# Kernel tuning notes

Hardware: AMD Instinct MI355X
Metric: run time of the kernel (lower is better)

The kernel has to match this reference:

```python
import jax, jax.numpy as jnp
import numpy as np

B, S, HID = 2, 2048, 2048
NH, NKV, HD = 16, 4, 128
GROUPS = NH // NKV
ROPE_BASE = 10000.0


def setup_inputs() -> dict:
    key = jax.random.key(0)
    ks = jax.random.split(key, 12)

    def w(k, i, o):
        return (jax.random.normal(k, (i, o), jnp.float32) * (i ** -0.5)).astype(jnp.float32)

    return {
        'x_real': jax.random.normal(ks[0], (B, S, HID), jnp.float32),
        'x_imag': jax.random.normal(ks[1], (B, S, HID), jnp.float32),
        'Wq_r': w(ks[2], HID, HID), 'Wq_i': w(ks[3], HID, HID),
        'bq_r': jnp.zeros((HID,), jnp.float32), 'bq_i': jnp.zeros((HID,), jnp.float32),
        'Wk_r': w(ks[4], HID, NKV * HD), 'Wk_i': w(ks[5], HID, NKV * HD),
        'bk_r': jnp.zeros((NKV * HD,), jnp.float32), 'bk_i': jnp.zeros((NKV * HD,), jnp.float32),
        'Wv_r': w(ks[6], HID, NKV * HD), 'Wv_i': w(ks[7], HID, NKV * HD),
        'bv_r': jnp.zeros((NKV * HD,), jnp.float32), 'bv_i': jnp.zeros((NKV * HD,), jnp.float32),
        'Wo_r': w(ks[8], HID, HID), 'Wo_i': w(ks[9], HID, HID),
        'bo_r': jnp.zeros((HID,), jnp.float32), 'bo_i': jnp.zeros((HID,), jnp.float32),
    }


def _clinear(xr, xi, Wr, Wi, br, bi):
    # complex linear: (xr + i*xi) @ (Wr + i*Wi) + (br + i*bi)
    out_r = xr @ Wr - xi @ Wi + br
    out_i = xr @ Wi + xi @ Wr + bi
    return out_r, out_i


def _split_heads(xr, xi, n_heads):
    b, s, _ = xr.shape
    xr = xr.reshape(b, s, n_heads, -1).transpose(0, 2, 1, 3)  # [B,H,S,D]
    xi = xi.reshape(b, s, n_heads, -1).transpose(0, 2, 1, 3)
    return xr, xi


def _rope(xr, xi):
    # complex rotary embedding: multiply (xr + i*xi) by exp(i * pos * inv_freq)
    s, d = xr.shape[-2], xr.shape[-1]
    inv_freq = 1.0 / (ROPE_BASE ** (jnp.arange(0, d, 2, dtype=jnp.float32) / d))
    freqs = jnp.arange(s, dtype=jnp.float32)[:, None] * inv_freq[None, :]  # [S, D/2]
    emb = jnp.concatenate([freqs, freqs], axis=-1)  # [S, D]
    cos, sin = jnp.cos(emb), jnp.sin(emb)
    return xr * cos - xi * sin, xr * sin + xi * cos


def _repeat_kv(xr, xi):
    if GROUPS == 1:
        return xr, xi
    b, hkv, s, d = xr.shape
    xr = jnp.broadcast_to(xr[:, :, None], (b, hkv, GROUPS, s, d)).reshape(b, NH, s, d)
    xi = jnp.broadcast_to(xi[:, :, None], (b, hkv, GROUPS, s, d)).reshape(b, NH, s, d)
    return xr, xi


def reference(x_real, x_imag, Wq_r, Wq_i, bq_r, bq_i, Wk_r, Wk_i, bk_r, bk_i,
              Wv_r, Wv_i, bv_r, bv_i, Wo_r, Wo_i, bo_r, bo_i):
    q_r, q_i = _clinear(x_real, x_imag, Wq_r, Wq_i, bq_r, bq_i)
    k_r, k_i = _clinear(x_real, x_imag, Wk_r, Wk_i, bk_r, bk_i)
    v_r, v_i = _clinear(x_real, x_imag, Wv_r, Wv_i, bv_r, bv_i)

    q_r, q_i = _split_heads(q_r, q_i, NH)
    k_r, k_i = _split_heads(k_r, k_i, NKV)
    v_r, v_i = _split_heads(v_r, v_i, NKV)

    q_r, q_i = _rope(q_r, q_i)
    k_r, k_i = _rope(k_r, k_i)

    k_r, k_i = _repeat_kv(k_r, k_i)
    v_r, v_i = _repeat_kv(v_r, v_i)

    scale = 1.0 / jnp.sqrt(jnp.float32(HD))
    # real part of complex inner product q . conj(k)
    scores = (jnp.einsum('bhqd,bhkd->bhqk', q_r, k_r)
              + jnp.einsum('bhqd,bhkd->bhqk', q_i, k_i)) * scale
    s = scores.shape[-1]
    causal = jnp.tril(jnp.ones((s, s), bool))
    scores = jnp.where(causal, scores, jnp.float32(-1e9))
    attn = jax.nn.softmax(scores, axis=-1)  # [B,H,S,S]

    out_r = jnp.einsum('bhqk,bhkd->bhqd', attn, v_r)
    out_i = jnp.einsum('bhqk,bhkd->bhqd', attn, v_i)

    # merge heads
    b = out_r.shape[0]
    out_r = out_r.transpose(0, 2, 1, 3).reshape(b, s, NH * HD)
    out_i = out_i.transpose(0, 2, 1, 3).reshape(b, s, NH * HD)

    out_r, out_i = _clinear(out_r, out_i, Wo_r, Wo_i, bo_r, bo_i)
    return out_r, out_i, attn
```

## Files before the change

kernel.cpp:

```cpp
#include <hip/hip_runtime.h>
#include <hip/hip_bf16.h>

#define S_LEN 2048
#define HIDDEN 2048
#define NHEAD 16
#define NKVH 4
#define HEADD 128
#define BATCH 2

typedef __attribute__((ext_vector_type(4))) float f32x4;
typedef __attribute__((ext_vector_type(8))) short bf16x8;
typedef __attribute__((ext_vector_type(4))) unsigned short u16x4;

__device__ __forceinline__ unsigned short f2bf(float f) {
  union { __hip_bfloat16 h; unsigned short u; } cv;
  cv.h = __float2bfloat16(f);
  return cv.u;
}

__device__ __forceinline__ float bf2f(unsigned short u) {
  union { float f; unsigned int i; } cv;
  cv.i = (unsigned int)u << 16;
  return cv.f;
}

__device__ __forceinline__ void gl_lds16(const void* g, void* l) {
  __builtin_amdgcn_global_load_lds(
      (const __attribute__((address_space(1))) unsigned int*)g,
      (__attribute__((address_space(3))) unsigned int*)l,
      16, 0, 0);
}

__device__ __forceinline__ f32x4 mfma16(bf16x8 a, bf16x8 b, f32x4 c) {
  return __builtin_amdgcn_mfma_f32_16x16x32_bf16(a, b, c, 0, 0, 0);
}

__global__ void k_rope_table(float* tab) {
  int idx = blockIdx.x * blockDim.x + threadIdx.x;
  if (idx >= S_LEN * 64) return;
  int s = idx >> 6, j = idx & 63;
  float invf = expf(-(float)j * (logf(10000.0f) / 64.0f));
  float ang = (float)s * invf;
  float sn, cs;
  sincosf(ang, &sn, &cs);
  tab[idx * 2 + 0] = cs;
  tab[idx * 2 + 1] = sn;
}

__global__ void k_pack_x(const float* __restrict__ xr, const float* __restrict__ xi,
                         unsigned short* __restrict__ Xp) {
  int idx = blockIdx.x * blockDim.x + threadIdx.x;
  if (idx >= 4096 * 4096 / 4) return;
  int m = idx >> 10;
  int c4 = idx & 1023;
  const float* src = (c4 < 512) ? (xr + (size_t)m * 2048 + c4 * 4)
                                : (xi + (size_t)m * 2048 + (c4 - 512) * 4);
  f32x4 v = *(const f32x4*)src;
  ((u16x4*)Xp)[idx] = (u16x4){f2bf(v.x), f2bf(v.y), f2bf(v.z), f2bf(v.w)};
}

__global__ void k_pack_w(const float* __restrict__ wq_r, const float* __restrict__ wq_i,
                         const float* __restrict__ wk_r, const float* __restrict__ wk_i,
                         const float* __restrict__ wv_r, const float* __restrict__ wv_i,
                         const float* __restrict__ wo_r, const float* __restrict__ wo_i,
                         unsigned short* __restrict__ Wt) {
  __shared__ float tile[32][33];
  int k0 = blockIdx.x * 32;
  int n0 = blockIdx.y * 32;
  int tx = threadIdx.x, ty0 = threadIdx.y;
#pragma unroll
  for (int i = 0; i < 4; ++i) {
    int ty = ty0 + i * 8;
    int k = k0 + ty;
    int n = n0 + tx;
    const float* Wr; const float* Wi; int w, part, j;
    if (n < 4096) {
      Wr = wq_r; Wi = wq_i; w = 2048;
      int h = n >> 8, p = (n >> 7) & 1, d = n & 127;
      part = p; j = h * 128 + d;
    } else if (n < 5120) {
      Wr = wk_r; Wi = wk_i; w = 512;
      int t = n - 4096;
      int kv = t >> 8, p = (t >> 7) & 1, d = t & 127;
      part = p; j = kv * 128 + d;
    } else if (n < 6144) {
      Wr = wv_r; Wi = wv_i; w = 512;
      int t = n - 5120;
      int kv = t >> 8, p = (t >> 7) & 1, d = t & 127;
      part = p; j = kv * 128 + d;
    } else {
      Wr = wo_r; Wi = wo_i; w = 2048;
      int t = n - 6144;
      part = (t >= w); j = part ? (t - w) : t;
    }
    float v;
    if (part == 0) v = (k < 2048) ? Wr[(size_t)k * w + j] : -Wi[(size_t)(k - 2048) * w + j];
    else           v = (k < 2048) ? Wi[(size_t)k * w + j] :  Wr[(size_t)(k - 2048) * w + j];
    tile[ty][tx] = v;
  }
  __syncthreads();
#pragma unroll
  for (int i = 0; i < 4; ++i) {
    int ty = ty0 + i * 8;
    Wt[(size_t)(n0 + ty) * 4096 + k0 + tx] = f2bf(tile[tx][ty]);
  }
}

template <int MODE>
__global__ __launch_bounds__(512, 2) void k_gemm256(
    const unsigned short* __restrict__ A, const unsigned short* __restrict__ Bt,
    int NTN,
    float* __restrict__ outR, float* __restrict__ outI,
    const float* __restrict__ bR, const float* __restrict__ bI,
    const float* __restrict__ tab,
    const float* __restrict__ bqr, const float* __restrict__ bqi,
    const float* __restrict__ bkr, const float* __restrict__ bki,
    const float* __restrict__ bvr, const float* __restrict__ bvi,
    unsigned short* __restrict__ Qcat, unsigned short* __restrict__ Kcat,
    unsigned short* __restrict__ VtP) {
  constexpr int KD = 4096;
  constexpr int Kb = KD * 2;
  constexpr int NT = KD / 64;
  constexpr int NITER = NT / 2;
  __shared__ __align__(16) char smem[131072];
  int tid = threadIdx.x, lane = tid & 63, wid = tid >> 6;
  int wm = wid >> 2, wn = wid & 3;
  int nwg = gridDim.x;
  int bid = blockIdx.x;
  int swz = (bid & 7) * (nwg >> 3) + (bid >> 3);
  int mt = swz / NTN, nt = swz - mt * NTN;
  int m0 = mt * 256, n0 = nt * 256;

  const char* Ab = (const char*)A + (size_t)m0 * Kb;
  const char* Bb = (const char*)Bt + (size_t)n0 * Kb;
  char* L = smem;

  int i0 = tid, i1 = tid + 512;
  int pl0 = (i0 >> 3) * Kb + (((i0 & 7) ^ ((i0 >> 3) & 7)) << 4);
  int pl1 = (i1 >> 3) * Kb + (((i1 & 7) ^ ((i1 >> 3) & 7)) << 4);

  int jx0 = (((lane >> 4)) ^ (lane & 7)) << 4;
  int jx1 = (((lane >> 4) + 4) ^ (lane & 7)) << 4;
  int arow = (wm * 64 + (lane & 15)) * 128;
  int brow = (wn * 32 + (lane & 15)) * 128;

  auto STAGE_A = [&](int buf, int half, int kt) {
    const char* s = Ab + (size_t)half * 128 * Kb + kt * 128;
    char* d = L + buf * 32768 + half * 16384 + (wid << 10);
    gl_lds16(s + pl0, d);
    gl_lds16(s + pl1, d + 8192);
  };
  auto STAGE_B = [&](int buf, int half, int kt) {
    const char* s = Bb + (size_t)half * 128 * Kb + kt * 128;
    char* d = L + 65536 + buf * 32768 + half * 16384 + (wid << 10);
    gl_lds16(s + pl0, d);
    gl_lds16(s + pl1, d + 8192);
  };
  auto LD_A = [&](bf16x8* dst, int buf, int half) {
    const char* base = L + buf * 32768 + half * 16384 + arow;
#pragma unroll
    for (int mf = 0; mf < 4; ++mf) {
      dst[mf * 2 + 0] = *(const bf16x8*)(base + mf * 2048 + jx0);
      dst[mf * 2 + 1] = *(const bf16x8*)(base + mf * 2048 + jx1);
    }
  };
  auto LD_B = [&](bf16x8* dst, int buf, int half) {
    const char* base = L + 65536 + buf * 32768 + half * 16384 + brow;
#pragma unroll
    for (int nf = 0; nf < 2; ++nf) {
      dst[nf * 2 + 0] = *(const bf16x8*)(base + nf * 2048 + jx0);
      dst[nf * 2 + 1] = *(const bf16x8*)(base + nf * 2048 + jx1);
    }
  };

  f32x4 acc[8][4];
  const f32x4 fz = {0.f, 0.f, 0.f, 0.f};
#pragma unroll
  for (int i = 0; i < 8; ++i)
#pragma unroll
    for (int j = 0; j < 4; ++j) acc[i][j] = fz;

  bf16x8 aX[8], aY[8], bX[4], bY[4];

#define BARR() __builtin_amdgcn_s_barrier()
#define WAITV(drain) do { if (drain) asm volatile("s_waitcnt vmcnt(0)" ::: "memory"); \
                          else       asm volatile("s_waitcnt vmcnt(6)" ::: "memory"); } while (0)
#define MMQ(aS, bS, qm, qn) do { \
    __builtin_amdgcn_s_setprio(1); \
    _Pragma("unroll") \
    for (int mf = 0; mf < 4; ++mf) \
      _Pragma("unroll") \
      for (int nf = 0; nf < 2; ++nf) { \
        acc[(qm)*4+mf][(qn)*2+nf] = mfma16(aS[mf*2+0], bS[nf*2+0], acc[(qm)*4+mf][(qn)*2+nf]); \
        acc[(qm)*4+mf][(qn)*2+nf] = mfma16(aS[mf*2+1], bS[nf*2+1], acc[(qm)*4+mf][(qn)*2+nf]); \
      } \
    __builtin_amdgcn_s_setprio(0); \
  } while (0)

  STAGE_A(0, 0, 0);
  STAGE_B(0, 0, 0);
  STAGE_B(0, 1, 0);
  STAGE_A(0, 1, 0);
  STAGE_A(1, 0, 1);
  STAGE_B(1, 0, 1);
  STAGE_B(1, 1, 1);
  asm volatile("s_waitcnt vmcnt(6)" ::: "memory");
  BARR();

  for (int it = 0; it < NITER; ++it) {
    int t1 = 2 * it + 1, t2 = 2 * it + 2, t3 = 2 * it + 3;
    bool nl = (it < NITER - 1);
    LD_A(aX, 0, 0); LD_B(bX, 0, 0);
    STAGE_A(1, 1, t1);
    BARR(); MMQ(aX, bX, 0, 0); BARR();
    LD_B(bY, 0, 1);
    if (nl) STAGE_A(0, 0, t2);
    BARR(); MMQ(aX, bY, 0, 1); BARR();
    LD_A(aY, 0, 1);
    if (nl) STAGE_B(0, 0, t2);
    BARR(); MMQ(aY, bY, 1, 1); BARR();
    if (nl) STAGE_B(0, 1, t2);
    WAITV(!nl); BARR(); MMQ(aY, bX, 1, 0); BARR();
    LD_A(aX, 1, 0); LD_B(bY, 1, 0);
    if (nl) STAGE_A(0, 1, t2);
    BARR(); MMQ(aX, bY, 0, 0); BARR();
    LD_B(bX, 1, 1);
    if (nl) STAGE_A(1, 0, t3);
    BARR(); MMQ(aX, bX, 0, 1); BARR();
    LD_A(aY, 1, 1);
    if (nl) STAGE_B(1, 0, t3);
    BARR(); MMQ(aY, bX, 1, 1); BARR();
    if (nl) STAGE_B(1, 1, t3);
    WAITV(!nl); BARR(); MMQ(aY, bY, 1, 0); BARR();
  }

  int r0 = (lane >> 4) << 2, col0 = lane & 15;

  if (MODE == 1) {
#pragma unroll
    for (int qm = 0; qm < 2; ++qm)
#pragma unroll
      for (int mf = 0; mf < 4; ++mf)
#pragma unroll
        for (int qn = 0; qn < 2; ++qn)
#pragma unroll
          for (int nf = 0; nf < 2; ++nf) {
            f32x4 v = acc[qm * 4 + mf][qn * 2 + nf];
            int rowb = m0 + qm * 128 + wm * 64 + mf * 16 + r0;
            int col = n0 + qn * 128 + wn * 32 + nf * 16 + col0;
#pragma unroll
            for (int r = 0; r < 4; ++r) {
              int row = rowb + r;
              if (col < 2048) outR[(size_t)row * 2048 + col] = v[r] + bR[col];
              else            outI[(size_t)row * 2048 + (col - 2048)] = v[r] + bI[col - 2048];
            }
          }
    return;
  }

  __syncthreads();
  int bidx = m0 >> 11;
  int s0 = m0 & 2047;

  if (n0 < 5120) {
    bool isQ = (n0 < 4096);
    int hh = isQ ? (n0 >> 8) : ((n0 - 4096) >> 8);
    const float* bRp = isQ ? bqr : bkr;
    const float* bIp = isQ ? bqi : bki;
    int jbase = hh * 128;
#pragma unroll
    for (int qm = 0; qm < 2; ++qm)
#pragma unroll
      for (int mf = 0; mf < 4; ++mf)
#pragma unroll
        for (int nf = 0; nf < 2; ++nf) {
          int d = wn * 32 + nf * 16 + col0;
          f32x4 vr = acc[qm * 4 + mf][0 * 2 + nf];
          f32x4 vi = acc[qm * 4 + mf][1 * 2 + nf];
          float br = bRp[jbase + d], bi = bIp[jbase + d];
#pragma unroll
          for (int r = 0; r < 4; ++r) {
            int lrow = qm * 128 + wm * 64 + mf * 16 + r0 + r;
            int s = s0 + lrow;
            float2 cs = *(const float2*)(tab + ((size_t)s * 64 + (d & 63)) * 2);
            float qr = vr[r] + br;
            float qi = vi[r] + bi;
            float orr = qr * cs.x - qi * cs.y;
            float oii = qr * cs.y + qi * cs.x;
            int swz4 = (lrow & 3) << 3;
            int g0 = (d >> 3) ^ swz4;
            int g1 = ((128 + d) >> 3) ^ swz4;
            *(unsigned short*)(L + lrow * 512 + g0 * 16 + (d & 7) * 2) = f2bf(orr);
            *(unsigned short*)(L + lrow * 512 + g1 * 16 + (d & 7) * 2) = f2bf(oii);
          }
        }
    __syncthreads();
    char* dstb = isQ ? (char*)Qcat + ((size_t)(bidx * 16 + hh) * 2048 + s0) * 512
                     : (char*)Kcat + ((size_t)(bidx * 4 + hh) * 2048 + s0) * 512;
#pragma unroll
    for (int i = 0; i < 16; ++i) {
      int cid = tid + 512 * i;
      int row = cid >> 5, c = cid & 31;
      int g = c ^ ((row & 3) << 3);
      *(f32x4*)(dstb + (size_t)row * 512 + c * 16) = *(const f32x4*)(L + row * 512 + g * 16);
    }
  } else {
    int kv = (n0 - 5120) >> 8;
#pragma unroll
    for (int qm = 0; qm < 2; ++qm)
#pragma unroll
      for (int mf = 0; mf < 4; ++mf)
#pragma unroll
        for (int qn = 0; qn < 2; ++qn)
#pragma unroll
          for (int nf = 0; nf < 2; ++nf) {
            int dloc = wn * 32 + nf * 16 + col0;
            int nlocal = qn * 128 + dloc;
            f32x4 v = acc[qm * 4 + mf][qn * 2 + nf];
            float bias = (qn ? bvi : bvr)[kv * 128 + dloc];
#pragma unroll
            for (int r = 0; r < 4; ++r) {
              int lrow = qm * 128 + wm * 64 + mf * 16 + r0 + r;
              int g = (lrow >> 3) ^ (nlocal & 31);
              *(unsigned short*)(L + nlocal * 512 + g * 16 + (lrow & 7) * 2) =
                  f2bf(v[r] + bias);
            }
          }
    __syncthreads();
    char* dstb = (char*)VtP + (size_t)(bidx * 4 + kv) * 256 * 4096 + (size_t)s0 * 2;
#pragma unroll
    for (int i = 0; i < 16; ++i) {
      int cid = tid + 512 * i;
      int n = cid >> 5, c = cid & 31;
      int g = c ^ (n & 31);
      *(f32x4*)(dstb + (size_t)n * 4096 + c * 16) = *(const f32x4*)(L + n * 512 + g * 16);
    }
  }
#undef BARR
#undef WAITV
#undef MMQ
}

__global__ __launch_bounds__(512, 1) void k_attn_fused(
    const unsigned short* __restrict__ Qcat, const unsigned short* __restrict__ Kcat,
    const unsigned short* __restrict__ Vt, float* __restrict__ attn,
    unsigned short* __restrict__ Cpack) {
  __shared__ __align__(16) char smem[148480];
  const float scale = 0.08838834764831845f;

  int tid = threadIdx.x, lane = tid & 63, wid = tid >> 6;
  int l15 = lane & 15, l4 = lane >> 4;
  int bid = blockIdx.x;
  int qt = 15 - (bid >> 5), bh = bid & 31;
  int b = bh >> 4, h = bh & 15;
  int nt = 2 * qt + 2;

  const char* Qb = (const char*)Qcat + (size_t)bh * S_LEN * 512 + (size_t)qt * 128 * 512;
  const char* Kb = (const char*)Kcat + (size_t)(b * NKVH + (h >> 2)) * S_LEN * 512;
  const char* Vb = (const char*)Vt + (size_t)(b * NKVH + (h >> 2)) * 256 * (size_t)S_LEN * 2;
  float* P = attn + (size_t)bh * S_LEN * S_LEN;

  int r5 = tid >> 5, c5 = tid & 31;
  int sw512 = ((c5 ^ (r5 & 7)) << 4);
  int r3 = tid >> 3, c3 = tid & 7;
  int sw128 = ((c3 ^ (r3 & 7)) << 4);
  char* ldst = smem + (wid << 10);

  auto stQ = [&]() {
#pragma unroll
    for (int c = 0; c < 8; ++c)
      gl_lds16(Qb + (size_t)(c * 16 + r5) * 512 + sw512, ldst + c * 8192);
  };
  auto stK = [&](int base, int kv0) {
#pragma unroll
    for (int c = 0; c < 4; ++c)
      gl_lds16(Kb + (size_t)(kv0 + c * 16 + r5) * 512 + sw512, ldst + base + c * 8192);
  };
  auto stV = [&](int kv0) {
#pragma unroll
    for (int c = 0; c < 4; ++c)
      gl_lds16(Vb + (size_t)(c * 64 + r3) * 4096 + kv0 * 2 + sw128,
               ldst + 98304 + c * 8192);
  };

  auto QKT = [&](f32x4 accs[2][2], int kbase) {
#pragma unroll
    for (int kf = 0; kf < 8; ++kf) {
      bf16x8 a[2], bb[2];
#pragma unroll
      for (int mf = 0; mf < 2; ++mf) {
        int row = (wid >> 1) * 32 + mf * 16 + l15;
        a[mf] = *(const bf16x8*)(smem + row * 512 + (((kf * 4 + l4) ^ (row & 7)) << 4));
      }
#pragma unroll
      for (int nf = 0; nf < 2; ++nf) {
        int row = (wid & 1) * 32 + nf * 16 + l15;
        bb[nf] = *(const bf16x8*)(smem + kbase + row * 512 + (((kf * 4 + l4) ^ (row & 7)) << 4));
      }
#pragma unroll
      for (int mf = 0; mf < 2; ++mf)
#pragma unroll
        for (int nf = 0; nf < 2; ++nf)
          accs[mf][nf] = mfma16(a[mf], bb[nf], accs[mf][nf]);
    }
  };

  float* sPart = (float*)(smem + 131072);
  float2* sML = (float2*)(smem + 147456);

#define BARL() do { asm volatile("s_waitcnt lgkmcnt(0)" ::: "memory"); \
                    __builtin_amdgcn_s_barrier(); } while (0)

  if (tid < 128) sML[tid] = make_float2(-1e30f, 0.f);
  stQ();
  stK(65536, 0);
  stK(98304, 64);
  asm volatile("s_waitcnt vmcnt(4)" ::: "memory");
  __builtin_amdgcn_s_barrier();

  for (int t = 0; t < nt; ++t) {
    int kbase = 65536 + (t & 1) * 32768;
    f32x4 accs[2][2];
#pragma unroll
    for (int i = 0; i < 2; ++i)
#pragma unroll
      for (int j = 0; j < 2; ++j) accs[i][j] = (f32x4){0.f, 0.f, 0.f, 0.f};
    QKT(accs, kbase);
    int kv0 = t * 64;
#pragma unroll
    for (int mf = 0; mf < 2; ++mf)
#pragma unroll
      for (int r = 0; r < 4; ++r) {
        int lrow = (wid >> 1) * 32 + mf * 16 + l4 * 4 + r;
        int grow = qt * 128 + lrow;
        int cA = kv0 + (wid & 1) * 32 + l15;
        float v0 = (cA <= grow) ? accs[mf][0][r] * scale : -1e30f;
        float v1 = (cA + 16 <= grow) ? accs[mf][1][r] * scale : -1e30f;
        float lm = fmaxf(v0, v1);
#pragma unroll
        for (int o = 1; o < 16; o <<= 1) lm = fmaxf(lm, __shfl_xor(lm, o));
        float ls = ((cA <= grow) ? __expf(v0 - lm) : 0.f) +
                   ((cA + 16 <= grow) ? __expf(v1 - lm) : 0.f);
#pragma unroll
        for (int o = 1; o < 16; o <<= 1) ls += __shfl_xor(ls, o);
        if (l15 == 0) {
          sPart[((wid & 1) * 128 + lrow) * 2 + 0] = lm;
          sPart[((wid & 1) * 128 + lrow) * 2 + 1] = ls;
        }
      }
    BARL();
    if (t + 2 < nt) stK(kbase, (t + 2) * 64);
    if (tid < 128) {
      float m0 = sPart[tid * 2], l0 = sPart[tid * 2 + 1];
      float m1 = sPart[(128 + tid) * 2], l1 = sPart[(128 + tid) * 2 + 1];
      float m01 = fmaxf(m0, m1);
      float l01 = l0 * __expf(m0 - m01) + l1 * __expf(m1 - m01);
      float2 old = sML[tid];
      float mn = fmaxf(old.x, m01);
      sML[tid] = make_float2(mn, old.y * __expf(old.x - mn) + l01 * __expf(m01 - mn));
    }
    BARL();
    if (t + 1 < nt) {
      if (t + 2 < nt) asm volatile("s_waitcnt vmcnt(4)" ::: "memory");
      else            asm volatile("s_waitcnt vmcnt(0)" ::: "memory");
      __builtin_amdgcn_s_barrier();
    }
  }
  if (tid < 128) {
    float2 ml = sML[tid];
    sML[tid] = make_float2(ml.x, 1.0f / ml.y);
  }
  BARL();

  stK(65536, 0);
  stV(0);
  asm volatile("s_waitcnt vmcnt(0)" ::: "memory");
  __builtin_amdgcn_s_barrier();

  int wmP = wid >> 2, wnP = wid & 3;
  f32x4 accp[4][4];
#pragma unroll
  for (int i = 0; i < 4; ++i)
#pragma unroll
    for (int j = 0; j < 4; ++j) accp[i][j] = (f32x4){0.f, 0.f, 0.f, 0.f};

  for (int t = 0; t < nt; ++t) {
    bool more = (t + 1 < nt);
    f32x4 accs[2][2];
#pragma unroll
    for (int i = 0; i < 2; ++i)
#pragma unroll
      for (int j = 0; j < 2; ++j) accs[i][j] = (f32x4){0.f, 0.f, 0.f, 0.f};
    QKT(accs, 65536);
    BARL();
    if (more) stK(65536, (t + 1) * 64);
    int kv0 = t * 64;
#pragma unroll
    for (int mf = 0; mf < 2; ++mf)
#pragma unroll
      for (int r = 0; r < 4; ++r) {
        int lrow = (wid >> 1) * 32 + mf * 16 + l4 * 4 + r;
        int grow = qt * 128 + lrow;
        float2 mi = sML[lrow];
#pragma unroll
        for (int nf = 0; nf < 2; ++nf) {
          int lcol = (wid & 1) * 32 + nf * 16 + l15;
          int gcol = kv0 + lcol;
          float s = accs[mf][nf][r] * scale;
          float p = (gcol <= grow) ? __expf(s - mi.x) * mi.y : 0.f;
          *(unsigned short*)(smem + 131072 + lrow * 128 +
                             (((lcol >> 3) ^ (lrow & 7)) << 4) + (lcol & 7) * 2) = f2bf(p);
        }
      }
    asm volatile("s_waitcnt lgkmcnt(0)" ::: "memory");
    if (more) asm volatile("s_waitcnt vmcnt(4)" ::: "memory");
    else      asm volatile("s_waitcnt vmcnt(0)" ::: "memory");
    __builtin_amdgcn_s_barrier();
#pragma unroll
    for (int p = 0; p < 4; ++p) {
      int row = p * 32 + wid * 4 + l4;
      int byte = 131072 + row * 128 + (((l15 >> 1) ^ (row & 7)) << 4) + (l15 & 1) * 8;
      u16x4 pv = *(const u16x4*)(smem + byte);
      f32x4 o = {bf2f(pv.x), bf2f(pv.y), bf2f(pv.z), bf2f(pv.w)};
      *(f32x4*)(P + (size_t)(qt * 128 + row) * S_LEN + kv0 + l15 * 4) = o;
    }
    __builtin_amdgcn_s_setprio(1);
#pragma unroll
    for (int ks = 0; ks < 2; ++ks) {
      bf16x8 a[4], bb[4];
#pragma unroll
      for (int mf = 0; mf < 4; ++mf) {
        int row = wmP * 64 + mf * 16 + l15;
        a[mf] = *(const bf16x8*)(smem + 131072 + row * 128 +
                                 (((ks * 4 + l4) ^ (row & 7)) << 4));
      }
#pragma unroll
      for (int nf = 0; nf < 4; ++nf) {
        int n = wnP * 64 + nf * 16 + l15;
        bb[nf] = *(const bf16x8*)(smem + 98304 + n * 128 +
                                  (((ks * 4 + l4) ^ (n & 7)) << 4));
      }
#pragma unroll
      for (int mf = 0; mf < 4; ++mf)
#pragma unroll
        for (int nf = 0; nf < 4; ++nf)
          accp[mf][nf] = mfma16(a[mf], bb[nf], accp[mf][nf]);
    }
    __builtin_amdgcn_s_setprio(0);
    BARL();
    if (more) {
      stV((t + 1) * 64);
      asm volatile("s_waitcnt vmcnt(8)" ::: "memory");
    }
    __builtin_amdgcn_s_barrier();
  }

  {
    int c0 = 128 * (qt + 1);
    const f32x4 z4 = {0.f, 0.f, 0.f, 0.f};
    for (int rr = 0; rr < 16; ++rr) {
      int grow = qt * 128 + wid * 16 + rr;
      for (int c = c0 + lane * 4; c < 2048; c += 256)
        *(f32x4*)(P + (size_t)grow * S_LEN + c) = z4;
    }
  }
  int r0w = l4 * 4;
#pragma unroll
  for (int mf = 0; mf < 4; ++mf)
#pragma unroll
    for (int nf = 0; nf < 4; ++nf) {
      int gmb = qt * 128 + wmP * 64 + mf * 16 + r0w;
      int nn = wnP * 64 + nf * 16 + l15;
      int gcol = (nn < 128) ? (h * 128 + nn) : (2048 + h * 128 + (nn - 128));
#pragma unroll
      for (int r = 0; r < 4; ++r)
        Cpack[(size_t)(b * S_LEN + gmb + r) * 4096 + gcol] = f2bf(accp[mf][nf][r]);
    }
#undef BARL
}

extern "C" void kernel_launch(void* const* d_in, const int* in_sizes, int n_in,
                              void* d_out, int out_size, void* d_ws, size_t ws_size,
                              hipStream_t stream) {
  const float* xr = (const float*)d_in[0];
  const float* xi = (const float*)d_in[1];
  const float* wq_r = (const float*)d_in[2];
  const float* wq_i = (const float*)d_in[3];
  const float* bq_r = (const float*)d_in[4];
  const float* bq_i = (const float*)d_in[5];
  const float* wk_r = (const float*)d_in[6];
  const float* wk_i = (const float*)d_in[7];
  const float* bk_r = (const float*)d_in[8];
  const float* bk_i = (const float*)d_in[9];
  const float* wv_r = (const float*)d_in[10];
  const float* wv_i = (const float*)d_in[11];
  const float* bv_r = (const float*)d_in[12];
  const float* bv_i = (const float*)d_in[13];
  const float* wo_r = (const float*)d_in[14];
  const float* wo_i = (const float*)d_in[15];
  const float* bo_r = (const float*)d_in[16];
  const float* bo_i = (const float*)d_in[17];

  float* out = (float*)d_out;
  float* outR = out;
  float* outI = out + (size_t)BATCH * S_LEN * HIDDEN;
  float* attn = outI + (size_t)BATCH * S_LEN * HIDDEN;

  char* ws = (char*)d_ws;
  size_t off = 0;
  auto alloc = [&](size_t bytes) {
    char* p = ws + off;
    off += (bytes + 255) & ~(size_t)255;
    return p;
  };
  unsigned short* Xp = (unsigned short*)alloc((size_t)4096 * 4096 * 2);
  unsigned short* Wt = (unsigned short*)alloc((size_t)10240 * 4096 * 2);
  float* tab = (float*)alloc((size_t)S_LEN * 64 * 2 * 4);
  unsigned short* Qcat = (unsigned short*)alloc((size_t)BATCH * NHEAD * S_LEN * 256 * 2);
  unsigned short* Kcat = (unsigned short*)alloc((size_t)BATCH * NKVH * S_LEN * 256 * 2);
  unsigned short* Vt = (unsigned short*)alloc((size_t)BATCH * NKVH * 256 * S_LEN * 2);
  unsigned short* Cpack = Xp;

  k_rope_table<<<512, 256, 0, stream>>>(tab);
  k_pack_x<<<16384, 256, 0, stream>>>(xr, xi, Xp);
  k_pack_w<<<dim3(128, 320), dim3(32, 8), 0, stream>>>(wq_r, wq_i, wk_r, wk_i, wv_r, wv_i,
                                                       wo_r, wo_i, Wt);
  k_gemm256<2><<<384, 512, 0, stream>>>(Xp, Wt, 24,
                                        nullptr, nullptr, nullptr, nullptr,
                                        tab, bq_r, bq_i, bk_r, bk_i, bv_r, bv_i,
                                        Qcat, Kcat, Vt);
  k_attn_fused<<<512, 512, 0, stream>>>(Qcat, Kcat, Vt, attn, Cpack);
  k_gemm256<1><<<256, 512, 0, stream>>>(Cpack, Wt + (size_t)6144 * 4096, 16,
                                        outR, outI, bo_r, bo_i,
                                        nullptr, nullptr, nullptr, nullptr, nullptr,
                                        nullptr, nullptr, nullptr, nullptr, nullptr);
}
```

Measured before the change: 729.5 us.

## Halve attention query tile to 64 rows and keep Q in registers

Shrinks the fused attention block's query tile from 128 to 64 rows and doubles the grid to 1024 blocks. Shared memory drops to about half, so launch bounds now ask for several blocks per CU, which raises occupancy and gives finer causal load balancing. The Q fragments are loaded once into registers instead of being re-read from LDS on every KV tile. In exchange, K and V tiles are fetched twice as often per query row, and register pressure under the tighter launch bound may cause spills.

```diff
diff --git a/kernel.cpp b/kernel.cpp
--- a/kernel.cpp
+++ b/kernel.cpp
@@ -341,21 +341,21 @@
 #undef MMQ
 }
 
-__global__ __launch_bounds__(512, 1) void k_attn_fused(
+__global__ __launch_bounds__(512, 4) void k_attn_fused(
     const unsigned short* __restrict__ Qcat, const unsigned short* __restrict__ Kcat,
     const unsigned short* __restrict__ Vt, float* __restrict__ attn,
     unsigned short* __restrict__ Cpack) {
-  __shared__ __align__(16) char smem[148480];
+  __shared__ __align__(16) char smem[74240];
   const float scale = 0.08838834764831845f;
 
   int tid = threadIdx.x, lane = tid & 63, wid = tid >> 6;
   int l15 = lane & 15, l4 = lane >> 4;
   int bid = blockIdx.x;
-  int qt = 15 - (bid >> 5), bh = bid & 31;
+  int qt = 31 - (bid >> 5), bh = bid & 31;
   int b = bh >> 4, h = bh & 15;
-  int nt = 2 * qt + 2;
-
-  const char* Qb = (const char*)Qcat + (size_t)bh * S_LEN * 512 + (size_t)qt * 128 * 512;
+  int nt = qt + 1;
+
+  const char* Qb = (const char*)Qcat + (size_t)bh * S_LEN * 512 + (size_t)qt * 64 * 512;
   const char* Kb = (const char*)Kcat + (size_t)(b * NKVH + (h >> 2)) * S_LEN * 512;
   const char* Vb = (const char*)Vt + (size_t)(b * NKVH + (h >> 2)) * 256 * (size_t)S_LEN * 2;
   float* P = attn + (size_t)bh * S_LEN * S_LEN;
@@ -368,7 +368,7 @@
 
   auto stQ = [&]() {
 #pragma unroll
-    for (int c = 0; c < 8; ++c)
+    for (int c = 0; c < 4; ++c)
       gl_lds16(Qb + (size_t)(c * 16 + r5) * 512 + sw512, ldst + c * 8192);
   };
   auto stK = [&](int base, int kv0) {
@@ -380,79 +380,79 @@
 #pragma unroll
     for (int c = 0; c < 4; ++c)
       gl_lds16(Vb + (size_t)(c * 64 + r3) * 4096 + kv0 * 2 + sw128,
-               ldst + 98304 + c * 8192);
-  };
-
-  auto QKT = [&](f32x4 accs[2][2], int kbase) {
+               ldst + 32768 + c * 8192);
+  };
+
+  float* sPart = (float*)(smem + 65536);
+  float2* sML = (float2*)(smem + 73728);
+
+#define BARL() do { asm volatile("s_waitcnt lgkmcnt(0)" ::: "memory"); \
+                    __builtin_amdgcn_s_barrier(); } while (0)
+
+  if (tid < 64) sML[tid] = make_float2(-1e30f, 0.f);
+  stQ();
+  asm volatile("s_waitcnt vmcnt(0)" ::: "memory");
+  __builtin_amdgcn_s_barrier();
+  bf16x8 q[8];
+  {
+    int row = (wid >> 1) * 16 + l15;
+#pragma unroll
+    for (int kf = 0; kf < 8; ++kf)
+      q[kf] = *(const bf16x8*)(smem + row * 512 + (((kf * 4 + l4) ^ (row & 7)) << 4));
+  }
+  BARL();
+
+  auto QKT = [&](f32x4 accs[2], int kbase) {
 #pragma unroll
     for (int kf = 0; kf < 8; ++kf) {
-      bf16x8 a[2], bb[2];
-#pragma unroll
-      for (int mf = 0; mf < 2; ++mf) {
-        int row = (wid >> 1) * 32 + mf * 16 + l15;
-        a[mf] = *(const bf16x8*)(smem + row * 512 + (((kf * 4 + l4) ^ (row & 7)) << 4));
-      }
+      bf16x8 bb[2];
 #pragma unroll
       for (int nf = 0; nf < 2; ++nf) {
         int row = (wid & 1) * 32 + nf * 16 + l15;
-        bb[nf] = *(const bf16x8*)(smem + kbase + row * 512 + (((kf * 4 + l4) ^ (row & 7)) << 4));
+        bb[nf] = *(const bf16x8*)(smem + kbase + row * 512 +
+                                  (((kf * 4 + l4) ^ (row & 7)) << 4));
       }
-#pragma unroll
-      for (int mf = 0; mf < 2; ++mf)
-#pragma unroll
-        for (int nf = 0; nf < 2; ++nf)
-          accs[mf][nf] = mfma16(a[mf], bb[nf], accs[mf][nf]);
-    }
-  };
-
-  float* sPart = (float*)(smem + 131072);
-  float2* sML = (float2*)(smem + 147456);
-
-#define BARL() do { asm volatile("s_waitcnt lgkmcnt(0)" ::: "memory"); \
-                    __builtin_amdgcn_s_barrier(); } while (0)
-
-  if (tid < 128) sML[tid] = make_float2(-1e30f, 0.f);
-  stQ();
-  stK(65536, 0);
-  stK(98304, 64);
+      accs[0] = mfma16(q[kf], bb[0], accs[0]);
+      accs[1] = mfma16(q[kf], bb[1], accs[1]);
+    }
+  };
+
+  stK(0, 0);
+  stK(32768, 64);
   asm volatile("s_waitcnt vmcnt(4)" ::: "memory");
   __builtin_amdgcn_s_barrier();
 
   for (int t = 0; t < nt; ++t) {
-    int kbase = 65536 + (t & 1) * 32768;
-    f32x4 accs[2][2];
-#pragma unroll
-    for (int i = 0; i < 2; ++i)
-#pragma unroll
-      for (int j = 0; j < 2; ++j) accs[i][j] = (f32x4){0.f, 0.f, 0.f, 0.f};
+    int kbase = (t & 1) * 32768;
+    f32x4 accs[2];
+    accs[0] = (f32x4){0.f, 0.f, 0.f, 0.f};
+    accs[1] = (f32x4){0.f, 0.f, 0.f, 0.f};
     QKT(accs, kbase);
     int kv0 = t * 64;
 #pragma unroll
-    for (int mf = 0; mf < 2; ++mf)
-#pragma unroll
-      for (int r = 0; r < 4; ++r) {
-        int lrow = (wid >> 1) * 32 + mf * 16 + l4 * 4 + r;
-        int grow = qt * 128 + lrow;
-        int cA = kv0 + (wid & 1) * 32 + l15;
-        float v0 = (cA <= grow) ? accs[mf][0][r] * scale : -1e30f;
-        float v1 = (cA + 16 <= grow) ? accs[mf][1][r] * scale : -1e30f;
-        float lm = fmaxf(v0, v1);
-#pragma unroll
-        for (int o = 1; o < 16; o <<= 1) lm = fmaxf(lm, __shfl_xor(lm, o));
-        float ls = ((cA <= grow) ? __expf(v0 - lm) : 0.f) +
-                   ((cA + 16 <= grow) ? __expf(v1 - lm) : 0.f);
-#pragma unroll
-        for (int o = 1; o < 16; o <<= 1) ls += __shfl_xor(ls, o);
-        if (l15 == 0) {
-          sPart[((wid & 1) * 128 + lrow) * 2 + 0] = lm;
-          sPart[((wid & 1) * 128 + lrow) * 2 + 1] = ls;
-        }
+    for (int r = 0; r < 4; ++r) {
+      int lrow = (wid >> 1) * 16 + l4 * 4 + r;
+      int grow = qt * 64 + lrow;
+      int cA = kv0 + (wid & 1) * 32 + l15;
+      float v0 = (cA <= grow) ? accs[0][r] * scale : -1e30f;
+      float v1 = (cA + 16 <= grow) ? accs[1][r] * scale : -1e30f;
+      float lm = fmaxf(v0, v1);
+#pragma unroll
+      for (int o = 1; o < 16; o <<= 1) lm = fmaxf(lm, __shfl_xor(lm, o));
+      float ls = ((cA <= grow) ? __expf(v0 - lm) : 0.f) +
+                 ((cA + 16 <= grow) ? __expf(v1 - lm) : 0.f);
+#pragma unroll
+      for (int o = 1; o < 16; o <<= 1) ls += __shfl_xor(ls, o);
+      if (l15 == 0) {
+        sPart[((wid & 1) * 64 + lrow) * 2 + 0] = lm;
+        sPart[((wid & 1) * 64 + lrow) * 2 + 1] = ls;
       }
+    }
     BARL();
     if (t + 2 < nt) stK(kbase, (t + 2) * 64);
-    if (tid < 128) {
+    if (tid < 64) {
       float m0 = sPart[tid * 2], l0 = sPart[tid * 2 + 1];
-      float m1 = sPart[(128 + tid) * 2], l1 = sPart[(128 + tid) * 2 + 1];
+      float m1 = sPart[(64 + tid) * 2], l1 = sPart[(64 + tid) * 2 + 1];
       float m01 = fmaxf(m0, m1);
       float l01 = l0 * __expf(m0 - m01) + l1 * __expf(m1 - m01);
       float2 old = sML[tid];
@@ -466,82 +466,80 @@
       __builtin_amdgcn_s_barrier();
     }
   }
-  if (tid < 128) {
+  if (tid < 64) {
     float2 ml = sML[tid];
     sML[tid] = make_float2(ml.x, 1.0f / ml.y);
   }
-  BARL();
-
-  stK(65536, 0);
+  asm volatile("s_waitcnt vmcnt(0) lgkmcnt(0)" ::: "memory");
+  __builtin_amdgcn_s_barrier();
+
+  stK(0, 0);
   stV(0);
   asm volatile("s_waitcnt vmcnt(0)" ::: "memory");
   __builtin_amdgcn_s_barrier();
 
   int wmP = wid >> 2, wnP = wid & 3;
-  f32x4 accp[4][4];
-#pragma unroll
-  for (int i = 0; i < 4; ++i)
+  f32x4 accp[2][4];
+#pragma unroll
+  for (int i = 0; i < 2; ++i)
 #pragma unroll
     for (int j = 0; j < 4; ++j) accp[i][j] = (f32x4){0.f, 0.f, 0.f, 0.f};
 
   for (int t = 0; t < nt; ++t) {
     bool more = (t + 1 < nt);
-    f32x4 accs[2][2];
-#pragma unroll
-    for (int i = 0; i < 2; ++i)
-#pragma unroll
-      for (int j = 0; j < 2; ++j) accs[i][j] = (f32x4){0.f, 0.f, 0.f, 0.f};
-    QKT(accs, 65536);
+    f32x4 accs[2];
+    accs[0] = (f32x4){0.f, 0.f, 0.f, 0.f};
+    accs[1] = (f32x4){0.f, 0.f, 0.f, 0.f};
+    QKT(accs, 0);
     BARL();
-    if (more) stK(65536, (t + 1) * 64);
+    if (more) stK(0, (t + 1) * 64);
     int kv0 = t * 64;
 #pragma unroll
-    for (int mf = 0; mf < 2; ++mf)
-#pragma unroll
-      for (int r = 0; r < 4; ++r) {
-        int lrow = (wid >> 1) * 32 + mf * 16 + l4 * 4 + r;
-        int grow = qt * 128 + lrow;
-        float2 mi = sML[lrow];
-#pragma unroll
-        for (int nf = 0; nf < 2; ++nf) {
-          int lcol = (wid & 1) * 32 + nf * 16 + l15;
-          int gcol = kv0 + lcol;
-          float s = accs[mf][nf][r] * scale;
-          float p = (gcol <= grow) ? __expf(s - mi.x) * mi.y : 0.f;
-          *(unsigned short*)(smem + 131072 + lrow * 128 +
-                             (((lcol >> 3) ^ (lrow & 7)) << 4) + (lcol & 7) * 2) = f2bf(p);
-        }
+    for (int r = 0; r < 4; ++r) {
+      int lrow = (wid >> 1) * 16 + l4 * 4 + r;
+      int grow = qt * 64 + lrow;
+      float2 mi = sML[lrow];
+#pragma unroll
+      for (int nf = 0; nf < 2; ++nf) {
+        int lcol = (wid & 1) * 32 + nf * 16 + l15;
+        int gcol = kv0 + lcol;
+        float s = accs[nf][r] * scale;
+        float p = (gcol <= grow) ? __expf(s - mi.x) * mi.y : 0.f;
+        *(unsigned short*)(smem + 65536 + lrow * 128 +
+                           (((lcol >> 3) ^ (lrow & 7)) << 4) + (lcol & 7) * 2) = f2bf(p);
       }
+    }
     asm volatile("s_waitcnt lgkmcnt(0)" ::: "memory");
     if (more) asm volatile("s_waitcnt vmcnt(4)" ::: "memory");
     else      asm volatile("s_waitcnt vmcnt(0)" ::: "memory");
     __builtin_amdgcn_s_barrier();
 #pragma unroll
-    for (int p = 0; p < 4; ++p) {
-      int row = p * 32 + wid * 4 + l4;
-      int byte = 131072 + row * 128 + (((l15 >> 1) ^ (row & 7)) << 4) + (l15 & 1) * 8;
+    for (int p = 0; p < 2; ++p) {
+      int idx = tid + 512 * p;
+      int row = idx >> 4, c16 = idx & 15;
+      int byte = 65536 + row * 128 + (((c16 >> 1) ^ (row & 7)) << 4) + (c16 & 1) * 8;
       u16x4 pv = *(const u16x4*)(smem + byte);
       f32x4 o = {bf2f(pv.x), bf2f(pv.y), bf2f(pv.z), bf2f(pv.w)};
-      *(f32x4*)(P + (size_t)(qt * 128 + row) * S_LEN + kv0 + l15 * 4) = o;
+      *(f32x4*)(P + (size_t)(qt * 64 + row) * S_LEN + kv0 + c16 * 4) = o;
     }
     __builtin_amdgcn_s_setprio(1);
 #pragma unroll
     for (int ks = 0; ks < 2; ++ks) {
-      bf16x8 a[4], bb[4];
-#pragma unroll
-      for (int mf = 0; mf < 4; ++mf) {
-        int row = wmP * 64 + mf * 16 + l15;
-        a[mf] = *(const bf16x8*)(smem + 131072 + row * 128 +
+      bf16x8 a[2], bb[4];
+#pragma unroll
+      for (int mf = 0; mf < 2; ++mf) {
+        int row = wmP * 32 + mf * 16 + l15;
+        a[mf] = *(const bf16x8*)(smem + 65536 + row * 128 +
                                  (((ks * 4 + l4) ^ (row & 7)) << 4));
       }
 #pragma unroll
       for (int nf = 0; nf < 4; ++nf) {
         int n = wnP * 64 + nf * 16 + l15;
-        bb[nf] = *(const bf16x8*)(smem + 98304 + n * 128 +
+        bb[nf] = *(const bf16x8*)(smem + 32768 + n * 128 +
                                   (((ks * 4 + l4) ^ (n & 7)) << 4));
       }
 #pragma unroll
-      for (int mf = 0; mf < 4; ++mf)
+      for (int mf = 0; mf < 2; ++mf)
 #pragma unroll
         for (int nf = 0; nf < 4; ++nf)
           accp[mf][nf] = mfma16(a[mf], bb[nf], accp[mf][nf]);
@@ -550,26 +548,26 @@
     BARL();
     if (more) {
       stV((t + 1) * 64);
-      asm volatile("s_waitcnt vmcnt(8)" ::: "memory");
+      asm volatile("s_waitcnt vmcnt(6)" ::: "memory");
     }
     __builtin_amdgcn_s_barrier();
   }
 
   {
-    int c0 = 128 * (qt + 1);
+    int c0 = 64 * (qt + 1);
     const f32x4 z4 = {0.f, 0.f, 0.f, 0.f};
-    for (int rr = 0; rr < 16; ++rr) {
-      int grow = qt * 128 + wid * 16 + rr;
+    for (int rr = 0; rr < 8; ++rr) {
+      int grow = qt * 64 + wid * 8 + rr;
       for (int c = c0 + lane * 4; c < 2048; c += 256)
         *(f32x4*)(P + (size_t)grow * S_LEN + c) = z4;
     }
   }
   int r0w = l4 * 4;
 #pragma unroll
-  for (int mf = 0; mf < 4; ++mf)
+  for (int mf = 0; mf < 2; ++mf)
 #pragma unroll
     for (int nf = 0; nf < 4; ++nf) {
-      int gmb = qt * 128 + wmP * 64 + mf * 16 + r0w;
+      int gmb = qt * 64 + wmP * 32 + mf * 16 + r0w;
       int nn = wnP * 64 + nf * 16 + l15;
       int gcol = (nn < 128) ? (h * 128 + nn) : (2048 + h * 128 + (nn - 128));
 #pragma unroll
@@ -629,7 +627,7 @@
                                         nullptr, nullptr, nullptr, nullptr,
                                         tab, bq_r, bq_i, bk_r, bk_i, bv_r, bv_i,
                                         Qcat, Kcat, Vt);
-  k_attn_fused<<<512, 512, 0, stream>>>(Qcat, Kcat, Vt, attn, Cpack);
+  k_attn_fused<<<1024, 512, 0, stream>>>(Qcat, Kcat, Vt, attn, Cpack);
   k_gemm256<1><<<256, 512, 0, stream>>>(Cpack, Wt + (size_t)6144 * 4096, 16,
                                         outR, outI, bo_r, bo_i,
                                         nullptr, nullptr, nullptr, nullptr, nullptr,
```

New measurement: 726.9 us. Within noise of the previous version (-0.4%).
